# Kernel optimization log

Hardware: AMD Instinct MI355X
Metric: run time of the kernel (lower is better)

Reference implementation:

```python
import math
import jax, jax.numpy as jnp
from jax import lax
import numpy as np

THETA = 10.0      # spiking threshold
TAU_SR = 10.0     # SRM (psp) alpha-kernel time constant
TAU_REF = 1.0     # refractory alpha-kernel time constant
SCALE_REF = 2.0   # refractory scale (kernel = -scaleRef*theta*alpha)
TAU_RHO = 1.0     # surrogate-gradient width
TS = 1.0          # simulation time step


def _alpha_filter_scan(x, tau, extra_input_fn=None):
    """Causal convolution along last (time) axis with alpha kernel
    k[n] = (n*Ts/tau) * exp(1 - n*Ts/tau)  (k[0] = 0),
    implemented exactly as a 2-state linear recurrence.
    x: [N, C, T] -> out: [N, C, T]."""
    d = jnp.float32(math.exp(-TS / tau))
    c = jnp.float32(math.e * TS / tau)
    xT = jnp.moveaxis(x, -1, 0)  # [T, N, C]

    def step(carry, xt):
        p, a = carry
        a = d * (a + p)          # alpha response from inputs up to t-1
        p = d * p + xt           # pure exponential state
        return (p, a), a * c

    z = jnp.zeros_like(xT[0])
    _, out = lax.scan(step, (z, z), xT)
    return jnp.moveaxis(out, 0, -1)


def psp(x):
    return _alpha_filter_scan(x, TAU_SR)


@jax.custom_vjp
def spike_fn(v):
    # Heaviside threshold on (membrane - theta)
    return (v >= 0).astype(v.dtype)

def _spike_fwd(v):
    return spike_fn(v), v

def _spike_bwd(v, g):
    # SLAYER surrogate gradient: exponential pdf around threshold
    grad = (1.0 / TAU_RHO) * jnp.exp(-jnp.abs(v) / TAU_RHO)
    return (g * grad,)

spike_fn.defvjp(_spike_fwd, _spike_bwd)


def spike_layer(u_in):
    """Threshold-and-refract over time. u_in: [N, C, T] psp potentials.
    Refractory response = -scaleRef*theta * alpha_{tauRef}(past spikes)."""
    d = jnp.float32(math.exp(-TS / TAU_REF))
    c = jnp.float32(math.e * TS / TAU_REF)
    ref_scale = jnp.float32(-SCALE_REF * THETA)
    uT = jnp.moveaxis(u_in, -1, 0)  # [T, N, C]

    def step(carry, ut):
        p, a = carry
        a = d * (a + p)                      # refractory potential at t
        u = ut + c * a                       # membrane potential
        s = spike_fn(u - THETA)              # spikes (0/1)
        p = d * p + ref_scale * s            # inject refractory impulse
        return (p, a), s

    z = jnp.zeros_like(uT[0])
    _, s = lax.scan(step, (z, z), uT)
    return jnp.moveaxis(s, 0, -1)


def setup_inputs() -> dict:
    key = jax.random.key(0)
    k1, k2, k3 = jax.random.split(key, 3)
    N, I, H, O, T = 64, 256, 1024, 18, 500
    # Bernoulli(0.1) input spikes
    spike_input = (jax.random.uniform(k1, (N, I, T)) < 0.1).astype(jnp.float32)
    W1 = jax.random.normal(k2, (H, I), dtype=jnp.float32) * (1.0 / math.sqrt(I))
    W2 = jax.random.normal(k3, (O, H), dtype=jnp.float32) * (1.0 / math.sqrt(H))
    return {"spike_input": spike_input, "W1": W1, "W2": W2}


def reference(spike_input, W1, W2):
    # layer 1: dense (per-timestep linear) -> psp -> spike
    y1 = jnp.einsum('nit,hi->nht', spike_input, W1)
    s1 = spike_layer(psp(y1))
    # layer 2
    y2 = jnp.einsum('nht,oh->not', s1, W2)
    s2 = spike_layer(psp(y2))
    return s2
```

## Files before the change

kernel.cpp:

```cpp
#include <hip/hip_runtime.h>
#include <hip/hip_bf16.h>


#define NN 64
#define II 256
#define HH 1024
#define OO 18
#define TT 500

#define D_SR 0.9048374180359595f
#define C_SR 0.27182818284590454f
#define D_RF 0.36787944117144233f
#define C_RF 2.718281828459045f
#define THETA 10.0f
#define REFS (-20.0f)

typedef _Float16 f16;
typedef _Float16 f16x2 __attribute__((ext_vector_type(2)));
typedef _Float16 f16x8 __attribute__((ext_vector_type(8)));
typedef float f32x4 __attribute__((ext_vector_type(4)));

__device__ __forceinline__ void gl2lds16(const void* g, void* l) {
    __builtin_amdgcn_global_load_lds(
        (const __attribute__((address_space(1))) void*)g,
        (__attribute__((address_space(3))) void*)l, 16, 0, 0);
}

__launch_bounds__(256)
__global__ void prep_x(const float* __restrict__ X, f16* __restrict__ Xb) {
    __shared__ float tile[64][65];
    const int n = blockIdx.z, i0 = blockIdx.y * 64, t0 = blockIdx.x * 64;
    const int tx = threadIdx.x & 63, q = threadIdx.x >> 6;
    const float* Xn = X + (size_t)n * II * TT;
#pragma unroll 4
    for (int j = 0; j < 16; ++j) {
        int il = j * 4 + q;
        int t = t0 + tx;
        tile[il][tx] = (t < TT) ? Xn[(size_t)(i0 + il) * TT + t] : 0.f;
    }
    __syncthreads();
#pragma unroll 4
    for (int j = 0; j < 16; ++j) {
        int tl = j * 4 + q;
        int t = t0 + tl;
        if (t < TT)
            Xb[((size_t)n * TT + t) * II + i0 + tx] = (f16)tile[tx][tl];
    }
}

__launch_bounds__(256)
__global__ void prep_w1(const float* __restrict__ W1, f16* __restrict__ Wh,
                        f16* __restrict__ Wl) {
    int idx = blockIdx.x * 256 + threadIdx.x;
    float w = W1[idx];
    f16 h = (f16)w;
    f16 l = (f16)(w - (float)h);
    Wh[idx] = h;
    Wl[idx] = l;
}

__launch_bounds__(256)
__global__ void prep_w2(const float* __restrict__ W2, f16* __restrict__ Wh,
                        f16* __restrict__ Wl) {
    int idx = blockIdx.x * 256 + threadIdx.x;
    int o = idx >> 10;
    float w = (o < OO) ? W2[idx] : 0.f;
    f16 h = (f16)w;
    f16 l = (f16)(w - (float)h);
    Wh[idx] = h;
    Wl[idx] = l;
}

__launch_bounds__(256)
__global__ void gemm1_scan1(const f16* __restrict__ Xb, const f16* __restrict__ Wh,
                            const f16* __restrict__ Wl, f16* __restrict__ S1) {
    __shared__ __align__(16) char smem[128 * 132 * 4];
    f16* As = (f16*)smem;
    f16* Bh = (f16*)(smem + 8192);
    f16* Bl = (f16*)(smem + 16384);
    float* yb = (float*)smem;

    const int tid = threadIdx.x;
    const int wave = tid >> 6, lane = tid & 63;

    const int f = blockIdx.y * 8 + blockIdx.x;
    const int x = f & 7, g = f >> 3;
    const int n = x * 8 + (g & 7);
    const int h0g = (g >> 3) * 128;

    const int rbl = wave * 32 + (lane >> 2);
    const f16* gBh0 = Wh + (size_t)(h0g + rbl) * II + (lane & 3) * 8;
    const f16* gBl0 = Wl + (size_t)(h0g + rbl) * II + (lane & 3) * 8;

    f16* lA0 = As + (wave * 32) * 32;
    f16* lA1 = lA0 + 16 * 32;
    f16* lBh0 = Bh + (wave * 32) * 32;
    f16* lBh1 = lBh0 + 16 * 32;
    f16* lBl0 = Bl + (wave * 32) * 32;
    f16* lBl1 = lBl0 + 16 * 32;

    const int wm = wave & 1, wn = wave >> 1;
    const int fr = lane & 15, kq = lane >> 4;

    float p1 = 0.f, a1 = 0.f, p2 = 0.f, a2 = 0.f;

    for (int c = 0; c < 4; ++c) {
        const int t0 = c * 128;
        const int TCe = (TT - t0 < 128) ? (TT - t0) : 128;

        int r0 = rbl;      if (r0 > TCe - 1) r0 = TCe - 1;
        int r1 = rbl + 16; if (r1 > TCe - 1) r1 = TCe - 1;
        const f16* gA0 = Xb + ((size_t)n * TT + t0 + r0) * II + (lane & 3) * 8;
        const f16* gA1 = Xb + ((size_t)n * TT + t0 + r1) * II + (lane & 3) * 8;

        f32x4 acc[4][4] = {};
        for (int kk = 0; kk < II / 32; ++kk) {
            const int ko = kk * 32;
            gl2lds16(gA0 + ko, lA0);
            gl2lds16(gA1 + ko, lA1);
            gl2lds16(gBh0 + ko, lBh0);
            gl2lds16(gBh0 + 16 * II + ko, lBh1);
            gl2lds16(gBl0 + ko, lBl0);
            gl2lds16(gBl0 + 16 * II + ko, lBl1);
            __syncthreads();

            f16x8 a[4], bh[4], bl[4];
#pragma unroll
            for (int i = 0; i < 4; ++i) {
                a[i]  = *(const f16x8*)(As + (wm * 64 + i * 16 + fr) * 32 + kq * 8);
                bh[i] = *(const f16x8*)(Bh + (wn * 64 + i * 16 + fr) * 32 + kq * 8);
                bl[i] = *(const f16x8*)(Bl + (wn * 64 + i * 16 + fr) * 32 + kq * 8);
            }
#pragma unroll
            for (int i = 0; i < 4; ++i)
#pragma unroll
                for (int j = 0; j < 4; ++j) {
                    acc[i][j] = __builtin_amdgcn_mfma_f32_16x16x32_f16(a[i], bh[j], acc[i][j], 0, 0, 0);
                    acc[i][j] = __builtin_amdgcn_mfma_f32_16x16x32_f16(a[i], bl[j], acc[i][j], 0, 0, 0);
                }
            __syncthreads();
        }

#pragma unroll
        for (int i = 0; i < 4; ++i)
#pragma unroll
            for (int j = 0; j < 4; ++j) {
                int tr = wm * 64 + i * 16 + kq * 4;
                int hc = wn * 64 + j * 16 + fr;
#pragma unroll
                for (int r = 0; r < 4; ++r)
                    yb[(tr + r) * 132 + hc] = acc[i][j][r];
            }
        __syncthreads();

        if (tid < 128) {
            float rb_[8];
#pragma unroll
            for (int j = 0; j < 8; ++j) rb_[j] = yb[j * 132 + tid];
            int t = 0;
            for (; t + 8 <= TCe; t += 8) {
#pragma unroll
                for (int j = 0; j < 8; ++j) {
                    float xv = rb_[j];
                    int tn = t + j + 8;
                    rb_[j] = (tn < TCe) ? yb[tn * 132 + tid] : 0.f;
                    a1 = D_SR * (a1 + p1);
                    p1 = D_SR * p1 + xv;
                    float ut = C_SR * a1;
                    a2 = D_RF * (a2 + p2);
                    float u = ut + C_RF * a2;
                    float s = (u >= THETA) ? 1.0f : 0.0f;
                    p2 = D_RF * p2 + REFS * s;
                    yb[(t + j) * 132 + tid] = s;
                }
            }
            int rem = TCe - t;
#pragma unroll
            for (int j = 0; j < 8; ++j) {
                if (j < rem) {
                    float xv = rb_[j];
                    a1 = D_SR * (a1 + p1);
                    p1 = D_SR * p1 + xv;
                    float ut = C_SR * a1;
                    a2 = D_RF * (a2 + p2);
                    float u = ut + C_RF * a2;
                    float s = (u >= THETA) ? 1.0f : 0.0f;
                    p2 = D_RF * p2 + REFS * s;
                    yb[(t + j) * 132 + tid] = s;
                }
            }
        }
        __syncthreads();

        const int rowq = tid >> 6;
#pragma unroll 4
        for (int pass = 0; pass < 32; ++pass) {
            int row = pass * 4 + rowq;
            if (row < TCe) {
                float v0 = yb[row * 132 + 2 * lane];
                float v1 = yb[row * 132 + 2 * lane + 1];
                f16x2 h2 = {(f16)v0, (f16)v1};
                *(f16x2*)(S1 + ((size_t)n * TT + t0 + row) * HH + h0g + 2 * lane) = h2;
            }
        }
        __syncthreads();
    }
}

__launch_bounds__(256)
__global__ void gemm2_mfma(const f16* __restrict__ S1, const f16* __restrict__ W2h,
                           const f16* __restrict__ W2l, float* __restrict__ Y2) {
    __shared__ __align__(16) f16 As[128 * 32];
    __shared__ __align__(16) f16 Bh[32 * 32];
    __shared__ __align__(16) f16 Bl[32 * 32];

    const int tid = threadIdx.x;
    const int wave = tid >> 6, lane = tid & 63;
    const int m0 = blockIdx.x * 128;

    const f16* gA0 = S1 + (size_t)(m0 + wave * 32 + (lane >> 2)) * HH + (lane & 3) * 8;
    const f16* gA1 = gA0 + (size_t)16 * HH;
    const f16* gB = (wave < 2 ? W2h : W2l) + (size_t)((wave & 1) * 16 + (lane >> 2)) * HH + (lane & 3) * 8;

    f16* lA0 = As + (wave * 32) * 32;
    f16* lA1 = lA0 + 16 * 32;
    f16* lB = (wave < 2 ? Bh : Bl) + ((wave & 1) * 16) * 32;

    f32x4 acc[2][2] = {};
    const int fr = lane & 15, kq = lane >> 4;

    for (int kk = 0; kk < HH / 32; ++kk) {
        const int ko = kk * 32;
        gl2lds16(gA0 + ko, lA0);
        gl2lds16(gA1 + ko, lA1);
        gl2lds16(gB + ko, lB);
        __syncthreads();

        f16x8 a[2], bh[2], bl[2];
#pragma unroll
        for (int i = 0; i < 2; ++i) {
            a[i]  = *(const f16x8*)(As + (wave * 32 + i * 16 + fr) * 32 + kq * 8);
            bh[i] = *(const f16x8*)(Bh + (i * 16 + fr) * 32 + kq * 8);
            bl[i] = *(const f16x8*)(Bl + (i * 16 + fr) * 32 + kq * 8);
        }
#pragma unroll
        for (int i = 0; i < 2; ++i)
#pragma unroll
            for (int j = 0; j < 2; ++j) {
                acc[i][j] = __builtin_amdgcn_mfma_f32_16x16x32_f16(a[i], bh[j], acc[i][j], 0, 0, 0);
                acc[i][j] = __builtin_amdgcn_mfma_f32_16x16x32_f16(a[i], bl[j], acc[i][j], 0, 0, 0);
            }
        __syncthreads();
    }

#pragma unroll
    for (int i = 0; i < 2; ++i)
#pragma unroll
        for (int j = 0; j < 2; ++j) {
            int rbase = m0 + wave * 32 + i * 16 + kq * 4;
            int cc = j * 16 + fr;
            float* p = Y2 + (size_t)rbase * 32 + cc;
#pragma unroll
            for (int r = 0; r < 4; ++r)
                p[(size_t)r * 32] = acc[i][j][r];
        }
}

#define PF2 16
__launch_bounds__(64)
__global__ void scan2_k(const float* __restrict__ Y2, float* __restrict__ Out) {
    __shared__ float sb[OO * TT];
    const int n = blockIdx.x, lane = threadIdx.x;
    const float* y = Y2 + (size_t)n * TT * 32;
    const bool act = (lane < 32);

    float p1 = 0.f, a1 = 0.f, p2 = 0.f, a2 = 0.f;
    float buf[PF2];
#pragma unroll
    for (int j = 0; j < PF2; ++j) buf[j] = act ? y[j * 32 + lane] : 0.f;

    int t = 0;
    for (; t + PF2 <= TT; t += PF2) {
#pragma unroll
        for (int j = 0; j < PF2; ++j) {
            float x = buf[j];
            buf[j] = (act && t + j + PF2 < TT) ? y[(t + j + PF2) * 32 + lane] : 0.f;
            a1 = D_SR * (a1 + p1);
            p1 = D_SR * p1 + x;
            float ut = C_SR * a1;
            a2 = D_RF * (a2 + p2);
            float u = ut + C_RF * a2;
            float s = (u >= THETA) ? 1.0f : 0.0f;
            p2 = D_RF * p2 + REFS * s;
            if (lane < OO) sb[lane * TT + t + j] = s;
        }
    }
#pragma unroll
    for (int j = 0; j < PF2; ++j) {
        if (t + j < TT) {
            float x = buf[j];
            a1 = D_SR * (a1 + p1);
            p1 = D_SR * p1 + x;
            float ut = C_SR * a1;
            a2 = D_RF * (a2 + p2);
            float u = ut + C_RF * a2;
            float s = (u >= THETA) ? 1.0f : 0.0f;
            p2 = D_RF * p2 + REFS * s;
            if (lane < OO) sb[lane * TT + t + j] = s;
        }
    }
    __syncthreads();
    float* on = Out + (size_t)n * OO * TT;
    for (int e = lane; e < OO * TT; e += 64) on[e] = sb[e];
}

extern "C" void kernel_launch(void* const* d_in, const int* in_sizes, int n_in,
                              void* d_out, int out_size, void* d_ws, size_t ws_size,
                              hipStream_t stream) {
    const float* X  = (const float*)d_in[0];
    const float* W1 = (const float*)d_in[1];
    const float* W2 = (const float*)d_in[2];
    float* out = (float*)d_out;

    const size_t s_s1b = (size_t)NN * TT * HH * 2;
    const size_t s_Xb  = (size_t)NN * TT * II * 2;
    const size_t s_W   = (size_t)HH * II * 2;
    const size_t s_W2  = (size_t)32 * HH * 2;

    char* w = (char*)d_ws;
    f16*   s1b = (f16*)w;                w += s_s1b;
    f16*   Xb  = (f16*)w;                w += s_Xb;
    f16*   W1h = (f16*)w;                w += s_W;
    f16*   W1l = (f16*)w;                w += s_W;
    f16*   W2h = (f16*)w;                w += s_W2;
    f16*   W2l = (f16*)w;                w += s_W2;
    float* y2  = (float*)w;

    prep_x<<<dim3(8, 4, NN), 256, 0, stream>>>(X, Xb);
    prep_w1<<<(HH * II) / 256, 256, 0, stream>>>(W1, W1h, W1l);
    prep_w2<<<(32 * HH) / 256, 256, 0, stream>>>(W2, W2h, W2l);

    gemm1_scan1<<<dim3(8, NN), 256, 0, stream>>>(Xb, W1h, W1l, s1b);

    gemm2_mfma<<<(NN * TT) / 128, 256, 0, stream>>>(s1b, W2h, W2l, y2);
    scan2_k<<<NN, 64, 0, stream>>>(y2, out);
}
```

Measured before the change: 217.5 us.

## Pre-tile GEMM operands into contiguous 128x32 fp16 blocks for coalesced LDS loads

The prep kernels now write X, W1 and W2, and the first GEMM writes its spike output S1, in a pre-tiled layout where each 128-row by 32-k block is stored contiguously. Each wave's global-to-LDS copy then reads one contiguous 1 KB span instead of strided rows, and the row clamping for the last time chunk goes away. The X transpose kernel now handles 128 time steps by 128 inputs per block, and the LDS stride for the scan buffer changes from 132 to 129. This adds index arithmetic to the prep kernels and to the S1 stores, which become scattered 4-byte writes into the tiled layout.

```diff
diff --git a/kernel.cpp b/kernel.cpp
--- a/kernel.cpp
+++ b/kernel.cpp
@@ -1,5 +1,4 @@
 #include <hip/hip_runtime.h>
-#include <hip/hip_bf16.h>
 
 
 #define NN 64
@@ -27,54 +26,87 @@
 }
 
 __launch_bounds__(256)
-__global__ void prep_x(const float* __restrict__ X, f16* __restrict__ Xb) {
-    __shared__ float tile[64][65];
-    const int n = blockIdx.z, i0 = blockIdx.y * 64, t0 = blockIdx.x * 64;
-    const int tx = threadIdx.x & 63, q = threadIdx.x >> 6;
-    const float* Xn = X + (size_t)n * II * TT;
+__global__ void prep_xt(const float* __restrict__ X, f16* __restrict__ Xt) {
+    __shared__ float tile[128 * 129];
+    const int c = blockIdx.x, n = blockIdx.y;
+    const int t0 = c * 128;
+    const int tid = threadIdx.x;
+    const int tx = tid & 63, rw = tid >> 6;
+    const int q = tid & 3, tl6 = tid >> 2;
+
+    for (int ih = 0; ih < 2; ++ih) {
+        const float* Xn = X + ((size_t)n * II + ih * 128) * TT;
 #pragma unroll 4
-    for (int j = 0; j < 16; ++j) {
-        int il = j * 4 + q;
-        int t = t0 + tx;
-        tile[il][tx] = (t < TT) ? Xn[(size_t)(i0 + il) * TT + t] : 0.f;
-    }
-    __syncthreads();
-#pragma unroll 4
-    for (int j = 0; j < 16; ++j) {
-        int tl = j * 4 + q;
-        int t = t0 + tl;
-        if (t < TT)
-            Xb[((size_t)n * TT + t) * II + i0 + tx] = (f16)tile[tx][tl];
-    }
-}
-
-__launch_bounds__(256)
-__global__ void prep_w1(const float* __restrict__ W1, f16* __restrict__ Wh,
-                        f16* __restrict__ Wl) {
+        for (int rep = 0; rep < 32; ++rep) {
+            int r = rep * 4 + rw;
+            int t = 2 * tx;
+            float v0 = 0.f, v1 = 0.f;
+            if (t0 + 128 <= TT) {
+                float2 v = *(const float2*)(Xn + (size_t)r * TT + t0 + t);
+                v0 = v.x; v1 = v.y;
+            } else {
+                if (t0 + t < TT)     v0 = Xn[(size_t)r * TT + t0 + t];
+                if (t0 + t + 1 < TT) v1 = Xn[(size_t)r * TT + t0 + t + 1];
+            }
+            tile[t * 129 + r] = v0;
+            tile[(t + 1) * 129 + r] = v1;
+        }
+        __syncthreads();
+#pragma unroll
+        for (int kkl = 0; kkl < 4; ++kkl)
+#pragma unroll
+            for (int hp = 0; hp < 2; ++hp) {
+                int row = hp * 64 + tl6;
+                f16x8 h;
+#pragma unroll
+                for (int e = 0; e < 8; ++e)
+                    h[e] = (f16)tile[row * 129 + kkl * 32 + q * 8 + e];
+                size_t dst = ((((size_t)(n * 4 + c) * 8 + ih * 4 + kkl) * 128 + row) * 32) + q * 8;
+                *(f16x8*)(Xt + dst) = h;
+            }
+        __syncthreads();
+    }
+}
+
+__launch_bounds__(256)
+__global__ void prep_w1t(const float* __restrict__ W1, f16* __restrict__ Wh,
+                         f16* __restrict__ Wl) {
     int idx = blockIdx.x * 256 + threadIdx.x;
-    float w = W1[idx];
-    f16 h = (f16)w;
-    f16 l = (f16)(w - (float)h);
-    Wh[idx] = h;
-    Wl[idx] = l;
-}
-
-__launch_bounds__(256)
-__global__ void prep_w2(const float* __restrict__ W2, f16* __restrict__ Wh,
-                        f16* __restrict__ Wl) {
+    int q = idx & 3, hl = (idx >> 2) & 127, kk = (idx >> 9) & 7, ht = idx >> 12;
+    const float* src = W1 + (size_t)(ht * 128 + hl) * II + kk * 32 + q * 8;
+    f16x8 h, l;
+#pragma unroll
+    for (int e = 0; e < 8; ++e) {
+        float w = src[e];
+        f16 hh = (f16)w;
+        h[e] = hh;
+        l[e] = (f16)(w - (float)hh);
+    }
+    *(f16x8*)(Wh + (size_t)idx * 8) = h;
+    *(f16x8*)(Wl + (size_t)idx * 8) = l;
+}
+
+__launch_bounds__(256)
+__global__ void prep_w2t(const float* __restrict__ W2, f16* __restrict__ Wh,
+                         f16* __restrict__ Wl) {
     int idx = blockIdx.x * 256 + threadIdx.x;
-    int o = idx >> 10;
-    float w = (o < OO) ? W2[idx] : 0.f;
-    f16 h = (f16)w;
-    f16 l = (f16)(w - (float)h);
-    Wh[idx] = h;
-    Wl[idx] = l;
-}
-
-__launch_bounds__(256)
-__global__ void gemm1_scan1(const f16* __restrict__ Xb, const f16* __restrict__ Wh,
-                            const f16* __restrict__ Wl, f16* __restrict__ S1) {
-    __shared__ __align__(16) char smem[128 * 132 * 4];
+    int q = idx & 3, o = (idx >> 2) & 31, kk = idx >> 7;
+    f16x8 h, l;
+#pragma unroll
+    for (int e = 0; e < 8; ++e) {
+        float w = (o < OO) ? W2[(size_t)o * HH + kk * 32 + q * 8 + e] : 0.f;
+        f16 hh = (f16)w;
+        h[e] = hh;
+        l[e] = (f16)(w - (float)hh);
+    }
+    *(f16x8*)(Wh + (size_t)idx * 8) = h;
+    *(f16x8*)(Wl + (size_t)idx * 8) = l;
+}
+
+__launch_bounds__(256)
+__global__ void gemm1_scan1(const f16* __restrict__ Xt, const f16* __restrict__ Wh,
+                            const f16* __restrict__ Wl, f16* __restrict__ S1sw) {
+    __shared__ __align__(16) char smem[128 * 129 * 4];
     f16* As = (f16*)smem;
     f16* Bh = (f16*)(smem + 8192);
     f16* Bl = (f16*)(smem + 16384);
@@ -86,18 +118,17 @@
     const int f = blockIdx.y * 8 + blockIdx.x;
     const int x = f & 7, g = f >> 3;
     const int n = x * 8 + (g & 7);
-    const int h0g = (g >> 3) * 128;
-
-    const int rbl = wave * 32 + (lane >> 2);
-    const f16* gBh0 = Wh + (size_t)(h0g + rbl) * II + (lane & 3) * 8;
-    const f16* gBl0 = Wl + (size_t)(h0g + rbl) * II + (lane & 3) * 8;
-
-    f16* lA0 = As + (wave * 32) * 32;
-    f16* lA1 = lA0 + 16 * 32;
-    f16* lBh0 = Bh + (wave * 32) * 32;
-    f16* lBh1 = lBh0 + 16 * 32;
-    f16* lBl0 = Bl + (wave * 32) * 32;
-    f16* lBl1 = lBl0 + 16 * 32;
+    const int ht = g >> 3;
+    const int h0g = ht * 128;
+
+    const f16* Abase = Xt + (size_t)(n * 4) * 8 * 4096;
+    const f16* Bhbase = Wh + (size_t)ht * 8 * 4096;
+    const f16* Blbase = Wl + (size_t)ht * 8 * 4096;
+    const int woff = wave * 1024 + lane * 8;
+
+    f16* lA = As + wave * 1024;
+    f16* lBh = Bh + wave * 1024;
+    f16* lBl = Bl + wave * 1024;
 
     const int wm = wave & 1, wn = wave >> 1;
     const int fr = lane & 15, kq = lane >> 4;
@@ -108,35 +139,32 @@
         const int t0 = c * 128;
         const int TCe = (TT - t0 < 128) ? (TT - t0) : 128;
 
-        int r0 = rbl;      if (r0 > TCe - 1) r0 = TCe - 1;
-        int r1 = rbl + 16; if (r1 > TCe - 1) r1 = TCe - 1;
-        const f16* gA0 = Xb + ((size_t)n * TT + t0 + r0) * II + (lane & 3) * 8;
-        const f16* gA1 = Xb + ((size_t)n * TT + t0 + r1) * II + (lane & 3) * 8;
-
         f32x4 acc[4][4] = {};
-        for (int kk = 0; kk < II / 32; ++kk) {
-            const int ko = kk * 32;
-            gl2lds16(gA0 + ko, lA0);
-            gl2lds16(gA1 + ko, lA1);
-            gl2lds16(gBh0 + ko, lBh0);
-            gl2lds16(gBh0 + 16 * II + ko, lBh1);
-            gl2lds16(gBl0 + ko, lBl0);
-            gl2lds16(gBl0 + 16 * II + ko, lBl1);
+        for (int kk = 0; kk < 8; ++kk) {
+            const f16* a = Abase + (size_t)(c * 8 + kk) * 4096 + woff;
+            const f16* bh = Bhbase + (size_t)kk * 4096 + woff;
+            const f16* bl = Blbase + (size_t)kk * 4096 + woff;
+            gl2lds16(a, lA);
+            gl2lds16(a + 512, lA + 512);
+            gl2lds16(bh, lBh);
+            gl2lds16(bh + 512, lBh + 512);
+            gl2lds16(bl, lBl);
+            gl2lds16(bl + 512, lBl + 512);
             __syncthreads();
 
-            f16x8 a[4], bh[4], bl[4];
+            f16x8 av[4], bhv[4], blv[4];
 #pragma unroll
             for (int i = 0; i < 4; ++i) {
-                a[i]  = *(const f16x8*)(As + (wm * 64 + i * 16 + fr) * 32 + kq * 8);
-                bh[i] = *(const f16x8*)(Bh + (wn * 64 + i * 16 + fr) * 32 + kq * 8);
-                bl[i] = *(const f16x8*)(Bl + (wn * 64 + i * 16 + fr) * 32 + kq * 8);
+                av[i]  = *(const f16x8*)(As + (wm * 64 + i * 16 + fr) * 32 + kq * 8);
+                bhv[i] = *(const f16x8*)(Bh + (wn * 64 + i * 16 + fr) * 32 + kq * 8);
+                blv[i] = *(const f16x8*)(Bl + (wn * 64 + i * 16 + fr) * 32 + kq * 8);
             }
 #pragma unroll
             for (int i = 0; i < 4; ++i)
 #pragma unroll
                 for (int j = 0; j < 4; ++j) {
-                    acc[i][j] = __builtin_amdgcn_mfma_f32_16x16x32_f16(a[i], bh[j], acc[i][j], 0, 0, 0);
-                    acc[i][j] = __builtin_amdgcn_mfma_f32_16x16x32_f16(a[i], bl[j], acc[i][j], 0, 0, 0);
+                    acc[i][j] = __builtin_amdgcn_mfma_f32_16x16x32_f16(av[i], bhv[j], acc[i][j], 0, 0, 0);
+                    acc[i][j] = __builtin_amdgcn_mfma_f32_16x16x32_f16(av[i], blv[j], acc[i][j], 0, 0, 0);
                 }
             __syncthreads();
         }
@@ -149,21 +177,21 @@
                 int hc = wn * 64 + j * 16 + fr;
 #pragma unroll
                 for (int r = 0; r < 4; ++r)
-                    yb[(tr + r) * 132 + hc] = acc[i][j][r];
+                    yb[(tr + r) * 129 + hc] = acc[i][j][r];
             }
         __syncthreads();
 
         if (tid < 128) {
             float rb_[8];
 #pragma unroll
-            for (int j = 0; j < 8; ++j) rb_[j] = yb[j * 132 + tid];
+            for (int j = 0; j < 8; ++j) rb_[j] = yb[j * 129 + tid];
             int t = 0;
             for (; t + 8 <= TCe; t += 8) {
 #pragma unroll
                 for (int j = 0; j < 8; ++j) {
                     float xv = rb_[j];
                     int tn = t + j + 8;
-                    rb_[j] = (tn < TCe) ? yb[tn * 132 + tid] : 0.f;
+                    rb_[j] = (tn < TCe) ? yb[tn * 129 + tid] : 0.f;
                     a1 = D_SR * (a1 + p1);
                     p1 = D_SR * p1 + xv;
                     float ut = C_SR * a1;
@@ -171,7 +199,7 @@
                     float u = ut + C_RF * a2;
                     float s = (u >= THETA) ? 1.0f : 0.0f;
                     p2 = D_RF * p2 + REFS * s;
-                    yb[(t + j) * 132 + tid] = s;
+                    yb[(t + j) * 129 + tid] = s;
                 }
             }
             int rem = TCe - t;
@@ -186,7 +214,7 @@
                     float u = ut + C_RF * a2;
                     float s = (u >= THETA) ? 1.0f : 0.0f;
                     p2 = D_RF * p2 + REFS * s;
-                    yb[(t + j) * 132 + tid] = s;
+                    yb[(t + j) * 129 + tid] = s;
                 }
             }
         }
@@ -197,18 +225,22 @@
         for (int pass = 0; pass < 32; ++pass) {
             int row = pass * 4 + rowq;
             if (row < TCe) {
-                float v0 = yb[row * 132 + 2 * lane];
-                float v1 = yb[row * 132 + 2 * lane + 1];
+                float v0 = yb[row * 129 + 2 * lane];
+                float v1 = yb[row * 129 + 2 * lane + 1];
+                int m = n * TT + t0 + row;
+                int mtile = m >> 7, ml = m & 127;
+                int h = h0g + 2 * lane;
+                int kk2 = h >> 5, hq = h & 31;
                 f16x2 h2 = {(f16)v0, (f16)v1};
-                *(f16x2*)(S1 + ((size_t)n * TT + t0 + row) * HH + h0g + 2 * lane) = h2;
-            }
-        }
-        __syncthreads();
-    }
-}
-
-__launch_bounds__(256)
-__global__ void gemm2_mfma(const f16* __restrict__ S1, const f16* __restrict__ W2h,
+                *(f16x2*)(S1sw + (((size_t)mtile * 32 + kk2) * 128 + ml) * 32 + hq) = h2;
+            }
+        }
+        __syncthreads();
+    }
+}
+
+__launch_bounds__(256)
+__global__ void gemm2_mfma(const f16* __restrict__ S1sw, const f16* __restrict__ W2h,
                            const f16* __restrict__ W2l, float* __restrict__ Y2) {
     __shared__ __align__(16) f16 As[128 * 32];
     __shared__ __align__(16) f16 Bh[32 * 32];
@@ -217,38 +249,34 @@
     const int tid = threadIdx.x;
     const int wave = tid >> 6, lane = tid & 63;
     const int m0 = blockIdx.x * 128;
-
-    const f16* gA0 = S1 + (size_t)(m0 + wave * 32 + (lane >> 2)) * HH + (lane & 3) * 8;
-    const f16* gA1 = gA0 + (size_t)16 * HH;
-    const f16* gB = (wave < 2 ? W2h : W2l) + (size_t)((wave & 1) * 16 + (lane >> 2)) * HH + (lane & 3) * 8;
-
-    f16* lA0 = As + (wave * 32) * 32;
-    f16* lA1 = lA0 + 16 * 32;
-    f16* lB = (wave < 2 ? Bh : Bl) + ((wave & 1) * 16) * 32;
+    const int fr = lane & 15, kq = lane >> 4;
+
+    f16* lA = As + wave * 1024;
+    f16* lB = (wave < 2 ? Bh : Bl) + (wave & 1) * 512;
 
     f32x4 acc[2][2] = {};
-    const int fr = lane & 15, kq = lane >> 4;
-
-    for (int kk = 0; kk < HH / 32; ++kk) {
-        const int ko = kk * 32;
-        gl2lds16(gA0 + ko, lA0);
-        gl2lds16(gA1 + ko, lA1);
-        gl2lds16(gB + ko, lB);
-        __syncthreads();
-
-        f16x8 a[2], bh[2], bl[2];
+
+    for (int kk = 0; kk < 32; ++kk) {
+        const f16* a = S1sw + ((size_t)blockIdx.x * 32 + kk) * 4096 + wave * 1024 + lane * 8;
+        gl2lds16(a, lA);
+        gl2lds16(a + 512, lA + 512);
+        const f16* bsrc = (wave < 2 ? W2h : W2l) + (size_t)kk * 1024 + (wave & 1) * 512 + lane * 8;
+        gl2lds16(bsrc, lB);
+        __syncthreads();
+
+        f16x8 av[2], bhv[2], blv[2];
 #pragma unroll
         for (int i = 0; i < 2; ++i) {
-            a[i]  = *(const f16x8*)(As + (wave * 32 + i * 16 + fr) * 32 + kq * 8);
-            bh[i] = *(const f16x8*)(Bh + (i * 16 + fr) * 32 + kq * 8);
-            bl[i] = *(const f16x8*)(Bl + (i * 16 + fr) * 32 + kq * 8);
+            av[i]  = *(const f16x8*)(As + (wave * 32 + i * 16 + fr) * 32 + kq * 8);
+            bhv[i] = *(const f16x8*)(Bh + (i * 16 + fr) * 32 + kq * 8);
+            blv[i] = *(const f16x8*)(Bl + (i * 16 + fr) * 32 + kq * 8);
         }
 #pragma unroll
         for (int i = 0; i < 2; ++i)
 #pragma unroll
             for (int j = 0; j < 2; ++j) {
-                acc[i][j] = __builtin_amdgcn_mfma_f32_16x16x32_f16(a[i], bh[j], acc[i][j], 0, 0, 0);
-                acc[i][j] = __builtin_amdgcn_mfma_f32_16x16x32_f16(a[i], bl[j], acc[i][j], 0, 0, 0);
+                acc[i][j] = __builtin_amdgcn_mfma_f32_16x16x32_f16(av[i], bhv[j], acc[i][j], 0, 0, 0);
+                acc[i][j] = __builtin_amdgcn_mfma_f32_16x16x32_f16(av[i], blv[j], acc[i][j], 0, 0, 0);
             }
         __syncthreads();
     }
@@ -322,26 +350,26 @@
     const float* W2 = (const float*)d_in[2];
     float* out = (float*)d_out;
 
-    const size_t s_s1b = (size_t)NN * TT * HH * 2;
-    const size_t s_Xb  = (size_t)NN * TT * II * 2;
-    const size_t s_W   = (size_t)HH * II * 2;
-    const size_t s_W2  = (size_t)32 * HH * 2;
+    const size_t s_s1 = (size_t)250 * 32 * 128 * 32 * 2;
+    const size_t s_Xt = (size_t)NN * 4 * 8 * 128 * 32 * 2;
+    const size_t s_W  = (size_t)8 * 8 * 128 * 32 * 2;
+    const size_t s_W2 = (size_t)32 * 32 * 32 * 2;
 
     char* w = (char*)d_ws;
-    f16*   s1b = (f16*)w;                w += s_s1b;
-    f16*   Xb  = (f16*)w;                w += s_Xb;
-    f16*   W1h = (f16*)w;                w += s_W;
-    f16*   W1l = (f16*)w;                w += s_W;
-    f16*   W2h = (f16*)w;                w += s_W2;
-    f16*   W2l = (f16*)w;                w += s_W2;
-    float* y2  = (float*)w;
-
-    prep_x<<<dim3(8, 4, NN), 256, 0, stream>>>(X, Xb);
-    prep_w1<<<(HH * II) / 256, 256, 0, stream>>>(W1, W1h, W1l);
-    prep_w2<<<(32 * HH) / 256, 256, 0, stream>>>(W2, W2h, W2l);
-
-    gemm1_scan1<<<dim3(8, NN), 256, 0, stream>>>(Xb, W1h, W1l, s1b);
-
-    gemm2_mfma<<<(NN * TT) / 128, 256, 0, stream>>>(s1b, W2h, W2l, y2);
+    f16*   s1sw = (f16*)w;  w += s_s1;
+    f16*   Xt   = (f16*)w;  w += s_Xt;
+    f16*   W1h  = (f16*)w;  w += s_W;
+    f16*   W1l  = (f16*)w;  w += s_W;
+    f16*   W2h  = (f16*)w;  w += s_W2;
+    f16*   W2l  = (f16*)w;  w += s_W2;
+    float* y2   = (float*)w;
+
+    prep_xt<<<dim3(4, NN), 256, 0, stream>>>(X, Xt);
+    prep_w1t<<<128, 256, 0, stream>>>(W1, W1h, W1l);
+    prep_w2t<<<16, 256, 0, stream>>>(W2, W2h, W2l);
+
+    gemm1_scan1<<<dim3(8, NN), 256, 0, stream>>>(Xt, W1h, W1l, s1sw);
+
+    gemm2_mfma<<<250, 256, 0, stream>>>(s1sw, W2h, W2l, y2);
     scan2_k<<<NN, 64, 0, stream>>>(y2, out);
 }
```

After: 244.2 us. 1.12x slower.

## Shrink gemm1_scan1 tiles to 64x64 and double the grid for more parallel scans

Applied to the files above, without the earlier changes.

The fused GEMM+scan kernel now uses 64-wide hidden tiles and 64-step time chunks instead of 128, with 1024 blocks instead of 512 and a launch-bounds occupancy hint of 4. Each block's sequential scan now runs on 64 threads over 64 steps per chunk. This spreads the serial scan work over twice as many blocks and raises occupancy through the smaller LDS footprint. In exchange, MFMA reuse per block drops and there are more barriers per unit of work.

```diff
diff --git a/kernel.cpp b/kernel.cpp
--- a/kernel.cpp
+++ b/kernel.cpp
@@ -1,5 +1,4 @@
 #include <hip/hip_runtime.h>
-#include <hip/hip_bf16.h>
 
 
 #define NN 64
@@ -71,99 +70,94 @@
     Wl[idx] = l;
 }
 
-__launch_bounds__(256)
+#define CT1 64
+__launch_bounds__(256, 4)
 __global__ void gemm1_scan1(const f16* __restrict__ Xb, const f16* __restrict__ Wh,
                             const f16* __restrict__ Wl, f16* __restrict__ S1) {
-    __shared__ __align__(16) char smem[128 * 132 * 4];
+    __shared__ __align__(16) char smem[CT1 * 66 * 4];
     f16* As = (f16*)smem;
-    f16* Bh = (f16*)(smem + 8192);
-    f16* Bl = (f16*)(smem + 16384);
+    f16* Bh = (f16*)(smem + 4096);
+    f16* Bl = (f16*)(smem + 8192);
     float* yb = (float*)smem;
 
     const int tid = threadIdx.x;
     const int wave = tid >> 6, lane = tid & 63;
 
-    const int f = blockIdx.y * 8 + blockIdx.x;
-    const int x = f & 7, g = f >> 3;
-    const int n = x * 8 + (g & 7);
-    const int h0g = (g >> 3) * 128;
-
-    const int rbl = wave * 32 + (lane >> 2);
-    const f16* gBh0 = Wh + (size_t)(h0g + rbl) * II + (lane & 3) * 8;
-    const f16* gBl0 = Wl + (size_t)(h0g + rbl) * II + (lane & 3) * 8;
-
-    f16* lA0 = As + (wave * 32) * 32;
-    f16* lA1 = lA0 + 16 * 32;
-    f16* lBh0 = Bh + (wave * 32) * 32;
-    f16* lBh1 = lBh0 + 16 * 32;
-    f16* lBl0 = Bl + (wave * 32) * 32;
-    f16* lBl1 = lBl0 + 16 * 32;
+    const int f = blockIdx.y * 16 + blockIdx.x;
+    const int xcd = f & 7, idx = f >> 3;
+    const int n = xcd * 8 + (idx & 7);
+    const int ht = idx >> 3;
+    const int h0g = ht * 64;
+
+    const int rloc = wave * 16 + (lane >> 2);
+    const int koff = (lane & 3) * 8;
+    const f16* gBh = Wh + (size_t)(h0g + rloc) * II + koff;
+    const f16* gBl = Wl + (size_t)(h0g + rloc) * II + koff;
+
+    f16* lA = As + wave * 512;
+    f16* lBh = Bh + wave * 512;
+    f16* lBl = Bl + wave * 512;
 
     const int wm = wave & 1, wn = wave >> 1;
     const int fr = lane & 15, kq = lane >> 4;
 
     float p1 = 0.f, a1 = 0.f, p2 = 0.f, a2 = 0.f;
 
-    for (int c = 0; c < 4; ++c) {
-        const int t0 = c * 128;
-        const int TCe = (TT - t0 < 128) ? (TT - t0) : 128;
-
-        int r0 = rbl;      if (r0 > TCe - 1) r0 = TCe - 1;
-        int r1 = rbl + 16; if (r1 > TCe - 1) r1 = TCe - 1;
-        const f16* gA0 = Xb + ((size_t)n * TT + t0 + r0) * II + (lane & 3) * 8;
-        const f16* gA1 = Xb + ((size_t)n * TT + t0 + r1) * II + (lane & 3) * 8;
-
-        f32x4 acc[4][4] = {};
-        for (int kk = 0; kk < II / 32; ++kk) {
+    for (int c = 0; c < 8; ++c) {
+        const int t0 = c * CT1;
+        const int TCe = (TT - t0 < CT1) ? (TT - t0) : CT1;
+
+        int ra = rloc; if (ra > TCe - 1) ra = TCe - 1;
+        const f16* gA = Xb + ((size_t)n * TT + t0 + ra) * II + koff;
+
+        f32x4 acc[2][2] = {};
+        for (int kk = 0; kk < 8; ++kk) {
             const int ko = kk * 32;
-            gl2lds16(gA0 + ko, lA0);
-            gl2lds16(gA1 + ko, lA1);
-            gl2lds16(gBh0 + ko, lBh0);
-            gl2lds16(gBh0 + 16 * II + ko, lBh1);
-            gl2lds16(gBl0 + ko, lBl0);
-            gl2lds16(gBl0 + 16 * II + ko, lBl1);
+            gl2lds16(gA + ko, lA);
+            gl2lds16(gBh + ko, lBh);
+            gl2lds16(gBl + ko, lBl);
             __syncthreads();
 
-            f16x8 a[4], bh[4], bl[4];
-#pragma unroll
-            for (int i = 0; i < 4; ++i) {
-                a[i]  = *(const f16x8*)(As + (wm * 64 + i * 16 + fr) * 32 + kq * 8);
-                bh[i] = *(const f16x8*)(Bh + (wn * 64 + i * 16 + fr) * 32 + kq * 8);
-                bl[i] = *(const f16x8*)(Bl + (wn * 64 + i * 16 + fr) * 32 + kq * 8);
-            }
-#pragma unroll
-            for (int i = 0; i < 4; ++i)
-#pragma unroll
-                for (int j = 0; j < 4; ++j) {
-                    acc[i][j] = __builtin_amdgcn_mfma_f32_16x16x32_f16(a[i], bh[j], acc[i][j], 0, 0, 0);
-                    acc[i][j] = __builtin_amdgcn_mfma_f32_16x16x32_f16(a[i], bl[j], acc[i][j], 0, 0, 0);
+            f16x8 av[2], bhv[2], blv[2];
+#pragma unroll
+            for (int i = 0; i < 2; ++i) {
+                av[i]  = *(const f16x8*)(As + (wm * 32 + i * 16 + fr) * 32 + kq * 8);
+                bhv[i] = *(const f16x8*)(Bh + (wn * 32 + i * 16 + fr) * 32 + kq * 8);
+                blv[i] = *(const f16x8*)(Bl + (wn * 32 + i * 16 + fr) * 32 + kq * 8);
+            }
+#pragma unroll
+            for (int i = 0; i < 2; ++i)
+#pragma unroll
+                for (int j = 0; j < 2; ++j) {
+                    acc[i][j] = __builtin_amdgcn_mfma_f32_16x16x32_f16(av[i], bhv[j], acc[i][j], 0, 0, 0);
+                    acc[i][j] = __builtin_amdgcn_mfma_f32_16x16x32_f16(av[i], blv[j], acc[i][j], 0, 0, 0);
                 }
             __syncthreads();
         }
 
 #pragma unroll
-        for (int i = 0; i < 4; ++i)
-#pragma unroll
-            for (int j = 0; j < 4; ++j) {
-                int tr = wm * 64 + i * 16 + kq * 4;
-                int hc = wn * 64 + j * 16 + fr;
+        for (int i = 0; i < 2; ++i)
+#pragma unroll
+            for (int j = 0; j < 2; ++j) {
+                int tr = wm * 32 + i * 16 + kq * 4;
+                int hc = wn * 32 + j * 16 + fr;
 #pragma unroll
                 for (int r = 0; r < 4; ++r)
-                    yb[(tr + r) * 132 + hc] = acc[i][j][r];
-            }
-        __syncthreads();
-
-        if (tid < 128) {
+                    yb[(tr + r) * 66 + hc] = acc[i][j][r];
+            }
+        __syncthreads();
+
+        if (tid < 64) {
             float rb_[8];
 #pragma unroll
-            for (int j = 0; j < 8; ++j) rb_[j] = yb[j * 132 + tid];
+            for (int j = 0; j < 8; ++j) rb_[j] = yb[j * 66 + tid];
             int t = 0;
             for (; t + 8 <= TCe; t += 8) {
 #pragma unroll
                 for (int j = 0; j < 8; ++j) {
                     float xv = rb_[j];
                     int tn = t + j + 8;
-                    rb_[j] = (tn < TCe) ? yb[tn * 132 + tid] : 0.f;
+                    rb_[j] = (tn < TCe) ? yb[tn * 66 + tid] : 0.f;
                     a1 = D_SR * (a1 + p1);
                     p1 = D_SR * p1 + xv;
                     float ut = C_SR * a1;
@@ -171,7 +165,7 @@
                     float u = ut + C_RF * a2;
                     float s = (u >= THETA) ? 1.0f : 0.0f;
                     p2 = D_RF * p2 + REFS * s;
-                    yb[(t + j) * 132 + tid] = s;
+                    yb[(t + j) * 66 + tid] = s;
                 }
             }
             int rem = TCe - t;
@@ -186,21 +180,21 @@
                     float u = ut + C_RF * a2;
                     float s = (u >= THETA) ? 1.0f : 0.0f;
                     p2 = D_RF * p2 + REFS * s;
-                    yb[(t + j) * 132 + tid] = s;
+                    yb[(t + j) * 66 + tid] = s;
                 }
             }
         }
         __syncthreads();
 
-        const int rowq = tid >> 6;
-#pragma unroll 4
-        for (int pass = 0; pass < 32; ++pass) {
-            int row = pass * 4 + rowq;
+#pragma unroll
+        for (int rep = 0; rep < 8; ++rep) {
+            int e = rep * 256 + tid;
+            int row = e >> 5, cp = e & 31;
             if (row < TCe) {
-                float v0 = yb[row * 132 + 2 * lane];
-                float v1 = yb[row * 132 + 2 * lane + 1];
+                float v0 = yb[row * 66 + 2 * cp];
+                float v1 = yb[row * 66 + 2 * cp + 1];
                 f16x2 h2 = {(f16)v0, (f16)v1};
-                *(f16x2*)(S1 + ((size_t)n * TT + t0 + row) * HH + h0g + 2 * lane) = h2;
+                *(f16x2*)(S1 + ((size_t)n * TT + t0 + row) * HH + h0g + 2 * cp) = h2;
             }
         }
         __syncthreads();
@@ -322,25 +316,25 @@
     const float* W2 = (const float*)d_in[2];
     float* out = (float*)d_out;
 
-    const size_t s_s1b = (size_t)NN * TT * HH * 2;
-    const size_t s_Xb  = (size_t)NN * TT * II * 2;
-    const size_t s_W   = (size_t)HH * II * 2;
-    const size_t s_W2  = (size_t)32 * HH * 2;
+    const size_t s_s1 = (size_t)NN * TT * HH * 2;
+    const size_t s_Xb = (size_t)NN * TT * II * 2;
+    const size_t s_W  = (size_t)HH * II * 2;
+    const size_t s_W2 = (size_t)32 * HH * 2;
 
     char* w = (char*)d_ws;
-    f16*   s1b = (f16*)w;                w += s_s1b;
-    f16*   Xb  = (f16*)w;                w += s_Xb;
-    f16*   W1h = (f16*)w;                w += s_W;
-    f16*   W1l = (f16*)w;                w += s_W;
-    f16*   W2h = (f16*)w;                w += s_W2;
-    f16*   W2l = (f16*)w;                w += s_W2;
+    f16*   s1b = (f16*)w;  w += s_s1;
+    f16*   Xb  = (f16*)w;  w += s_Xb;
+    f16*   W1h = (f16*)w;  w += s_W;
+    f16*   W1l = (f16*)w;  w += s_W;
+    f16*   W2h = (f16*)w;  w += s_W2;
+    f16*   W2l = (f16*)w;  w += s_W2;
     float* y2  = (float*)w;
 
     prep_x<<<dim3(8, 4, NN), 256, 0, stream>>>(X, Xb);
     prep_w1<<<(HH * II) / 256, 256, 0, stream>>>(W1, W1h, W1l);
     prep_w2<<<(32 * HH) / 256, 256, 0, stream>>>(W2, W2h, W2l);
 
-    gemm1_scan1<<<dim3(8, NN), 256, 0, stream>>>(Xb, W1h, W1l, s1b);
+    gemm1_scan1<<<dim3(16, NN), 256, 0, stream>>>(Xb, W1h, W1l, s1b);
 
     gemm2_mfma<<<(NN * TT) / 128, 256, 0, stream>>>(s1b, W2h, W2l, y2);
     scan2_k<<<NN, 64, 0, stream>>>(y2, out);
```

Result: slower. 223.4 us (+2.7%).
